# Kernel optimization log

Hardware: AMD Instinct MI355X
Metric: run time of the kernel (lower is better)

## Reference

```python
import jax, jax.numpy as jnp
import numpy as np

B, C, T, H, W = 1, 512, 8, 48, 48
GROUPS = 32
EPS = 1e-6


def setup_inputs() -> dict:
    key = jax.random.key(0)
    ks = jax.random.split(key, 6)
    s = 0.02  # init scale for projection weights
    return {
        "x": jax.random.normal(ks[0], (B, C, T, H, W), dtype=jnp.float32),
        "gamma": jnp.ones((C,), dtype=jnp.float32),
        "beta": jnp.zeros((C,), dtype=jnp.float32),
        "wq": jax.random.normal(ks[1], (C, C), dtype=jnp.float32) * s,
        "bq": jnp.zeros((C,), dtype=jnp.float32),
        "wk": jax.random.normal(ks[2], (C, C), dtype=jnp.float32) * s,
        "bk": jnp.zeros((C,), dtype=jnp.float32),
        "wv": jax.random.normal(ks[3], (C, C), dtype=jnp.float32) * s,
        "bv": jnp.zeros((C,), dtype=jnp.float32),
        "wo": jax.random.normal(ks[4], (C, C), dtype=jnp.float32) * s,
        "bo": jnp.zeros((C,), dtype=jnp.float32),
    }


def _group_norm(x, gamma, beta):
    b, c, t, h, w = x.shape
    xg = x.reshape(b, GROUPS, c // GROUPS, t, h, w)
    mu = xg.mean(axis=(2, 3, 4, 5), keepdims=True)
    var = xg.var(axis=(2, 3, 4, 5), keepdims=True)
    xn = ((xg - mu) * jax.lax.rsqrt(var + EPS)).reshape(b, c, t, h, w)
    return xn * gamma[None, :, None, None, None] + beta[None, :, None, None, None]


def _proj(h, wgt, bias):
    # CausalConv3d with kernel_size=1 == pointwise channel linear
    return jnp.einsum('oc,bcthw->bothw', wgt, h) + bias[None, :, None, None, None]


def reference(x, gamma, beta, wq, bq, wk, bk, wv, bv, wo, bo):
    hn = _group_norm(x, gamma, beta)
    q = _proj(hn, wq, bq)
    k = _proj(hn, wk, bk)
    v = _proj(hn, wv, bv)
    b, c, t, h, w = q.shape
    n = h * w
    # per-frame spatial attention: (b, t, n, c)
    qf = q.transpose(0, 2, 3, 4, 1).reshape(b, t, n, c)
    kf = k.transpose(0, 2, 3, 4, 1).reshape(b, t, n, c)
    vf = v.transpose(0, 2, 3, 4, 1).reshape(b, t, n, c)
    scores = jnp.einsum('btqc,btkc->btqk', qf, kf) * (c ** -0.5)
    attn = jax.nn.softmax(scores, axis=-1)
    of = jnp.einsum('btqk,btkc->btqc', attn, vf)
    o = of.reshape(b, t, h, w, c).transpose(0, 4, 1, 2, 3)
    o = _proj(o, wo, bo)
    return x + o
```

## Files before the change

### kernel.cpp

```cpp
#include <hip/hip_runtime.h>
#include <hip/hip_bf16.h>
#include <cstdint>
#include <type_traits>

typedef __attribute__((ext_vector_type(8))) __bf16 bf16x8;
typedef __attribute__((ext_vector_type(4))) float f32x4;
typedef __attribute__((ext_vector_type(2))) long longx2;

struct bf2frag { bf16x8 k0, k1; };

__device__ __forceinline__ float bf2f(unsigned short u) {
  union { uint32_t i; float f; } v; v.i = (uint32_t)u << 16; return v.f;
}
__device__ __forceinline__ unsigned short f2bf(float f) {
  union { float f; uint32_t i; } v{f};
  uint32_t r = v.i + 0x7fffu + ((v.i >> 16) & 1u);
  return (unsigned short)(r >> 16);
}

__device__ __forceinline__ void gll(const void* g, void* l) {
  __builtin_amdgcn_global_load_lds(
      (const __attribute__((address_space(1))) uint32_t*)(uintptr_t)g,
      (__attribute__((address_space(3))) uint32_t*)(uint32_t)(uintptr_t)l,
      16, 0, 0);
}

__device__ __forceinline__ void bar() {
  asm volatile("" ::: "memory");
  __builtin_amdgcn_s_barrier();
  asm volatile("" ::: "memory");
}

#define VMCNT(n) asm volatile("s_waitcnt vmcnt(" #n ")" ::: "memory")

template <int N>
__device__ __forceinline__ void vmw() {
  if constexpr (N == 0) { VMCNT(0); }
  else if constexpr (N == 1) { VMCNT(1); }
  else if constexpr (N == 2) { VMCNT(2); }
  else if constexpr (N == 3) { VMCNT(3); }
  else if constexpr (N == 4) { VMCNT(4); }
  else if constexpr (N == 5) { VMCNT(5); }
  else if constexpr (N == 6) { VMCNT(6); }
  else if constexpr (N == 7) { VMCNT(7); }
  else if constexpr (N == 8) { VMCNT(8); }
  else if constexpr (N == 9) { VMCNT(9); }
  else if constexpr (N == 10) { VMCNT(10); }
  else { VMCNT(12); }
}

__device__ __forceinline__ f32x4 mma(bf16x8 a, bf16x8 b, f32x4 c) {
  return __builtin_amdgcn_mfma_f32_16x16x32_bf16(a, b, c, 0, 0, 0);
}
__device__ __forceinline__ f32x4 mma(long a, long b, f32x4 c) {
  return __builtin_amdgcn_mfma_f32_16x16x32_fp8_fp8(a, b, c, 0, 0, 0);
}
__device__ __forceinline__ f32x4 mmak(const bf2frag& a, const bf2frag& b, f32x4 c, int k2) {
  return k2 ? mma(a.k1, b.k1, c) : mma(a.k0, b.k0, c);
}
__device__ __forceinline__ f32x4 mmak(longx2 a, longx2 b, f32x4 c, int k2) {
  return mma(a[k2], b[k2], c);
}

__device__ __forceinline__ int perm64(int m) {
  return (m & ~63) | (((m >> 3) & 3) << 4) | (((m >> 5) & 1) << 3) | (m & 7);
}

__global__ __launch_bounds__(256) void stats_partial_k(const float* __restrict__ x,
                                                       float* __restrict__ part) {
  const int g = blockIdx.x >> 3, p = blockIdx.x & 7;
  const float* base = x + (long)g * 16 * 18432 + (long)p * 2304;
  float s = 0.f, ss = 0.f;
  for (int idx = threadIdx.x; idx < 16 * 576; idx += 256) {
    const int c = idx / 576, i4 = idx % 576;
    const float4 v = *(const float4*)(base + (long)c * 18432 + i4 * 4);
    s += v.x + v.y + v.z + v.w;
    ss += v.x * v.x + v.y * v.y + v.z * v.z + v.w * v.w;
  }
  __shared__ float rs[256], rss[256];
  rs[threadIdx.x] = s; rss[threadIdx.x] = ss;
  __syncthreads();
  for (int o = 128; o > 0; o >>= 1) {
    if ((int)threadIdx.x < o) { rs[threadIdx.x] += rs[threadIdx.x + o]; rss[threadIdx.x] += rss[threadIdx.x + o]; }
    __syncthreads();
  }
  if (threadIdx.x == 0) { part[blockIdx.x * 2] = rs[0]; part[blockIdx.x * 2 + 1] = rss[0]; }
}

__global__ __launch_bounds__(256) void gn_transpose_k(const float* __restrict__ x,
                                                      const float* __restrict__ part,
                                                      const float* __restrict__ gamma,
                                                      const float* __restrict__ beta,
                                                      unsigned short* __restrict__ hnT) {
  __shared__ float tile[64][65];
  __shared__ float sm[4], sr[4];
  const int c0 = blockIdx.x * 64, n0 = blockIdx.y * 64;
  const int tn = threadIdx.x & 63, tr = threadIdx.x >> 6;
  if (threadIdx.x < 4) {
    const int g = (c0 >> 4) + threadIdx.x;
    float s = 0.f, ss = 0.f;
    for (int p = 0; p < 8; ++p) { s += part[(g * 8 + p) * 2]; ss += part[(g * 8 + p) * 2 + 1]; }
    const float mean = s / 294912.0f;
    const float var = ss / 294912.0f - mean * mean;
    sm[threadIdx.x] = mean;
    sr[threadIdx.x] = rsqrtf(var + 1e-6f);
  }
  __syncthreads();
  for (int cc = tr; cc < 64; cc += 4) {
    const int c = c0 + cc;
    const float mean = sm[cc >> 4], rstd = sr[cc >> 4];
    const float v = x[(long)c * 18432 + n0 + tn];
    tile[cc][tn] = (v - mean) * rstd * gamma[c] + beta[c];
  }
  __syncthreads();
  for (int nn = tr; nn < 64; nn += 4) {
    hnT[(long)(n0 + nn) * 512 + c0 + tn] = f2bf(tile[tn][nn]);
  }
}

__global__ __launch_bounds__(256) void pack4_bf16_k(const float* __restrict__ w0,
                                                    const float* __restrict__ w1,
                                                    const float* __restrict__ w2,
                                                    const float* __restrict__ w3,
                                                    unsigned short* __restrict__ o0,
                                                    unsigned short* __restrict__ o1,
                                                    unsigned short* __restrict__ o2,
                                                    unsigned short* __restrict__ o3,
                                                    const float* __restrict__ bq,
                                                    const float* __restrict__ bk,
                                                    float* __restrict__ bqk) {
  const int y = blockIdx.y;
  if (y == 4) {
    if (blockIdx.x == 0) {
      const int i = threadIdx.x * 4;
#pragma unroll
      for (int j = 0; j < 4; ++j) {
        const int t = i + j;
        bqk[t] = (t < 512) ? bq[t] : bk[t - 512];
      }
    }
    return;
  }
  const float* w = (y == 0) ? w0 : (y == 1) ? w1 : (y == 2) ? w2 : w3;
  unsigned short* o = (y == 0) ? o0 : (y == 1) ? o1 : (y == 2) ? o2 : o3;
  const int i = (blockIdx.x * 256 + threadIdx.x) * 4;
  const float4 v = *(const float4*)(w + i);
  ushort4 u; u.x = f2bf(v.x); u.y = f2bf(v.y); u.z = f2bf(v.z); u.w = f2bf(v.w);
  *(ushort4*)(o + i) = u;
}

template <int BM, int BIAS_MODE, int OUT_MODE, int STATS, int SCALEN, int MODE, int FP8, int P2,
          int WL = 0, int KU = 1>
__global__ __launch_bounds__((BM == 256) ? 512 : 256, (WL && FP8) ? (KU == 2 ? 2 : 4) : 2)
void gemm256(const void* __restrict__ A, long lda, long sAz,
             const void* __restrict__ B, long ldb, long sBz,
             void* __restrict__ Cp, long ldc, long sCz,
             const float* __restrict__ bias,
             const float* __restrict__ resid,
             float* __restrict__ rowsums,
             const float* __restrict__ linv,
             float alpha, int K, int gx, int gy) {
  static_assert(KU == 1 || FP8, "KU=2 only on fp8 path");
  constexpr int EB = FP8 ? 1 : 2;
  constexpr int THREADS = (BM == 256) ? 512 : 256;
  constexpr int BN = WL ? 128 : 256;
  constexpr int BK = 64 * KU;
  constexpr int HBA = (BM / 2) * BK * EB;
  constexpr int HBB = (BN / 2) * BK * EB;
  constexpr int HBA0 = HBA / KU, HBB0 = HBB / KU;
  constexpr int GA = HBA / (THREADS * 16);
  constexpr int GB = HBB / (THREADS * 16);
  constexpr int GA0 = GA / KU, GB0 = GB / KU;
  constexpr int V0 = GB + 2 * GA, V3 = 2 * GB + GA, VP = GB + GA;
  constexpr int NSLOT = WL ? 8 : ((BM == 256) ? 8 : 4);
  constexpr int NSLOTP = NSLOT + 1;
  constexpr int MR = WL ? 4 : 8;
  constexpr int FQ = WL ? 2 : 4;
  constexpr int PRIO = !P2;
  __shared__ alignas(16) unsigned char As[2][2][HBA];
  __shared__ alignas(16) unsigned char Bs[2][2][HBB];
  __shared__ float linvs[SCALEN == 2 ? BN : 1];
  using ABt2 = typename std::conditional<FP8, longx2, bf2frag>::type;

  const int tid = threadIdx.x;
  const int lane = tid & 63, wid = tid >> 6;
  const int wm = WL ? (wid >> 1) : ((BM == 256) ? (wid & 1) : 0);
  const int wn = WL ? (wid & 1) : ((BM == 256) ? (wid >> 1) : wid);
  int bx, by, bz;
  const void* Asel = A;
  const void* Bsel = B;
  void* Csel = Cp;
  const float* biasSel = bias;
  long ldcSel = ldc;
  bool bias_m = (BIAS_MODE == 1);
  {
    const int g8 = blockIdx.x & 7, n = blockIdx.x >> 3;
    if (MODE == 0) { bz = g8; bx = n % gx; by = n / gx; }
    else if (MODE == 1) { bz = 0; bx = n % gx; by = g8 * gy + n / gx; }
    else if (MODE == 2) { bz = 0; by = n % gy; bx = g8 * gx + n / gy; }
    else {
      bz = 0;
      if ((int)blockIdx.x < gx) {
        bx = n % 8; by = g8 * 18 + n / 8;
      } else {
        const int b2 = (int)blockIdx.x - gx;
        const int g82 = b2 & 7, n2 = b2 >> 3;
        by = n2 % 4; bx = g82 * 18 + n2 / 4;
        Asel = B;
        Bsel = (const void*)resid;
        Csel = (void*)rowsums;
        biasSel = linv;
        ldcSel = 18432;
        bias_m = false;
      }
    }
  }
  const unsigned char* Ab = (const unsigned char*)Asel + ((long)bz * sAz + (long)bx * BM * lda) * EB;
  const unsigned char* Bb = (const unsigned char*)Bsel + ((long)bz * sBz + (long)by * BN * ldb) * EB;

  if constexpr (SCALEN == 2) {
    if (tid < BN) {
      const int ntile = K / BN;
      float L = 0.f;
      for (int xx = 0; xx < ntile; ++xx)
        L += rowsums[((long)(bz * ntile + xx)) * K + by * BN + tid];
      linvs[tid] = 1.0f / L;
    }
  }

  auto stageA = [&](int slot, int h, int k0) {
    if constexpr (!FP8) {
      const int ksw = ((tid & 7) << 3) ^ (((tid >> 3) & 7) << 3);
#pragma unroll
      for (int call = 0; call < GA; ++call) {
        const int r = call * (THREADS / 8) + (tid >> 3);
        const int grow = WL ? (((r >> 5) << 6) + h * 32 + (r & 31))
                            : (((r >> 6) << 7) + h * 64 + (r & 63));
        gll(Ab + ((long)grow * lda + k0) * 2 + ksw * 2, &As[slot][h][call * THREADS * 16 + tid * 16]);
      }
    } else {
#pragma unroll
      for (int call = 0; call < GA; ++call) {
        const int sub = call / GA0, c0 = call % GA0;
        const int l = c0 * (THREADS / 4) + (tid >> 2);
        const int grow = WL ? (((l >> 5) << 6) + h * 32 + (l & 31))
                            : (((l >> 6) << 7) + h * 64 + (l & 63));
        const int x = (((l & 3) ^ ((l >> 2) & 3)) << 4);
        gll(Ab + (long)grow * lda + k0 + sub * 64 + (((tid & 3) << 4) ^ x),
            &As[slot][h][call * THREADS * 16 + tid * 16]);
      }
    }
  };
  auto stageB = [&](int slot, int h, int k0) {
    if constexpr (!FP8) {
      const int ksw = ((tid & 7) << 3) ^ (((tid >> 3) & 7) << 3);
#pragma unroll
      for (int call = 0; call < GB; ++call) {
        const int r = call * (THREADS / 8) + (tid >> 3);
        const int grow = ((r >> 5) << 6) + h * 32 + (r & 31);
        gll(Bb + ((long)grow * ldb + k0) * 2 + ksw * 2, &Bs[slot][h][call * THREADS * 16 + tid * 16]);
      }
    } else {
#pragma unroll
      for (int call = 0; call < GB; ++call) {
        const int sub = call / GB0, c0 = call % GB0;
        const int l = c0 * (THREADS / 4) + (tid >> 2);
        const int grow = ((l >> 5) << 6) + h * 32 + (l & 31);
        const int x = (((l & 3) ^ ((l >> 2) & 3)) << 4);
        gll(Bb + (long)grow * ldb + k0 + sub * 64 + (((tid & 3) << 4) ^ x),
            &Bs[slot][h][call * THREADS * 16 + tid * 16]);
      }
    }
  };
  auto ldA = [&](int slot, int mh, int fq, int sub) -> ABt2 {
    const int r = (WL ? wm * 32 : wm * 64) + fq * 16 + (lane & 15);
    if constexpr (!FP8) {
      bf2frag f;
      const int kk0 = (((lane >> 4) << 3)) ^ ((r & 7) << 3);
      const int kk1 = (32 + ((lane >> 4) << 3)) ^ ((r & 7) << 3);
      f.k0 = *reinterpret_cast<const bf16x8*>(&As[slot][mh][r * 128 + kk0 * 2]);
      f.k1 = *reinterpret_cast<const bf16x8*>(&As[slot][mh][r * 128 + kk1 * 2]);
      return f;
    } else {
      const int x = (((r & 3) ^ ((r >> 2) & 3)) << 4);
      const int kk = ((lane >> 4) << 4) ^ x;
      return *reinterpret_cast<const longx2*>(&As[slot][mh][sub * HBA0 + r * 64 + kk]);
    }
  };
  auto ldB = [&](int slot, int nh, int g, int sub) -> ABt2 {
    const int r = wn * 32 + g * 16 + (lane & 15);
    if constexpr (!FP8) {
      bf2frag f;
      const int kk0 = (((lane >> 4) << 3)) ^ ((r & 7) << 3);
      const int kk1 = (32 + ((lane >> 4) << 3)) ^ ((r & 7) << 3);
      f.k0 = *reinterpret_cast<const bf16x8*>(&Bs[slot][nh][r * 128 + kk0 * 2]);
      f.k1 = *reinterpret_cast<const bf16x8*>(&Bs[slot][nh][r * 128 + kk1 * 2]);
      return f;
    } else {
      const int x = (((r & 3) ^ ((r >> 2) & 3)) << 4);
      const int kk = ((lane >> 4) << 4) ^ x;
      return *reinterpret_cast<const longx2*>(&Bs[slot][nh][sub * HBB0 + r * 64 + kk]);
    }
  };

  f32x4 acc[MR][4] = {};
  ABt2 a[FQ * KU], b0[2 * KU], b1[2 * KU];

#define READ_A(SLOT, MH)                                                       \
  _Pragma("unroll") for (int fq = 0; fq < FQ; ++fq)                            \
    _Pragma("unroll") for (int sub = 0; sub < KU; ++sub)                       \
      a[fq * KU + sub] = ldA(SLOT, MH, fq, sub);
#define READ_B(SLOT, NH, DST)                                                  \
  _Pragma("unroll") for (int g = 0; g < 2; ++g)                                \
    _Pragma("unroll") for (int sub = 0; sub < KU; ++sub)                       \
      DST[g * KU + sub] = ldB(SLOT, NH, g, sub);
#define MFMA_QUAD(MH, NH, BARR)                                                \
  if constexpr (PRIO) __builtin_amdgcn_s_setprio(1);                           \
  _Pragma("unroll") for (int fq = 0; fq < FQ; ++fq)                            \
    _Pragma("unroll") for (int g = 0; g < 2; ++g)                              \
      _Pragma("unroll") for (int sub = 0; sub < KU; ++sub)                     \
        _Pragma("unroll") for (int k2 = 0; k2 < 2; ++k2)                       \
          acc[(MH) * FQ + fq][(NH) * 2 + g] =                                  \
              mmak(a[fq * KU + sub], BARR[g * KU + sub],                       \
                   acc[(MH) * FQ + fq][(NH) * 2 + g], k2);                     \
  if constexpr (PRIO) __builtin_amdgcn_s_setprio(0);

  const int KT = K / BK;
  stageB(0, 0, 0);
  stageA(0, 0, 0);
  stageB(0, 1, 0);
  stageA(0, 1, 0);
  stageB(1, 0, BK);
  if constexpr (!P2) stageA(1, 1, BK);
  vmw<VP>();
  bar();

  if constexpr (!P2) {
    for (int W = 0; W < KT; ++W) {
      const int s = W & 1;
      const int kn1 = (W + 1) * BK, kn2 = (W + 2) * BK;
      const bool st1 = (W + 1 < KT), st2 = (W + 2 < KT);
      READ_A(s, 0)
      READ_B(s, 0, b0)
      if (st1) stageA(s ^ 1, 0, kn1);
      bar();
      MFMA_QUAD(0, 0, b0)
      if (st1) { vmw<V0>(); }
      bar();
      READ_B(s, 1, b1)
      if (st1) stageB(s ^ 1, 1, kn1);
      bar();
      MFMA_QUAD(0, 1, b1)
      bar();
      READ_A(s, 1)
      if (st2) stageB(s, 0, kn2);
      bar();
      MFMA_QUAD(1, 1, b1)
      bar();
      if (st2) stageA(s, 1, kn2);
      bar();
      MFMA_QUAD(1, 0, b0)
      if (st2) { vmw<V3>(); } else { vmw<0>(); }
      bar();
    }
  } else {
    for (int W = 0; W < KT; ++W) {
      const int s = W & 1;
      const int kn1 = (W + 1) * BK, kn2 = (W + 2) * BK;
      const bool st1 = (W + 1 < KT), st2 = (W + 2 < KT);
      READ_A(s, 0)
      READ_B(s, 0, b0)
      READ_B(s, 1, b1)
      if (st1) { stageA(s ^ 1, 0, kn1); stageB(s ^ 1, 1, kn1); stageA(s ^ 1, 1, kn1); }
      bar();
      MFMA_QUAD(0, 0, b0)
      MFMA_QUAD(0, 1, b1)
      if (st1) { vmw<2 * (GA + GB)>(); } else { vmw<0>(); }
      bar();
      READ_A(s, 1)
      if (st2) stageB(s, 0, kn2);
      bar();
      MFMA_QUAD(1, 1, b1)
      MFMA_QUAD(1, 0, b0)
      if (st2) { vmw<GA + GB>(); } else if (st1) { vmw<GA>(); } else { vmw<0>(); }
      bar();
    }
  }

  const int mg0 = bx * BM + (WL ? wm * 64 : wm * 128) + ((lane >> 4) << 2);
  const int ng0 = by * BN + wn * 64 + (lane & 15);
  float* red = (float*)&As[0][0][0];
#pragma unroll
  for (int N = 0; N < 4; ++N) {
    const int n = ng0 + (N >> 1) * 32 + (N & 1) * 16;
    float bn;
    if constexpr (MODE == 3) bn = bias_m ? 0.f : biasSel[n];
    else bn = (BIAS_MODE == 2) ? bias[n] : 0.f;
    const float sc = (SCALEN == 1) ? linv[(long)bz * 2304 + n]
                   : (SCALEN == 2) ? linvs[n - by * BN] : 1.0f;
    float eN = 0.f;
#pragma unroll
    for (int M = 0; M < MR; ++M) {
      const int m = mg0 + (WL ? ((M >> 1) * 32 + (M & 1) * 16) : ((M >> 2) * 64 + (M & 3) * 16));
      const f32x4 av = acc[M][N];
      float vals[4];
#pragma unroll
      for (int j = 0; j < 4; ++j) {
        float addv;
        if constexpr (MODE == 3) addv = bias_m ? biasSel[m + j] : bn;
        else if constexpr (BIAS_MODE == 1) addv = bias[m + j];
        else addv = bn;
        vals[j] = av[j] * alpha + addv;
        if (SCALEN) vals[j] *= sc;
        if (STATS) { vals[j] = __expf(vals[j]); eN += vals[j]; }
      }
      if (OUT_MODE == 0) {
        ushort4 o; o.x = f2bf(vals[0]); o.y = f2bf(vals[1]); o.z = f2bf(vals[2]); o.w = f2bf(vals[3]);
        *(ushort4*)((unsigned short*)Csel + (long)bz * sCz + (long)n * ldcSel + m) = o;
      } else if (OUT_MODE == 2) {
        int pk = __builtin_amdgcn_cvt_pk_fp8_f32(vals[0], vals[1], 0, false);
        pk = __builtin_amdgcn_cvt_pk_fp8_f32(vals[2], vals[3], pk, true);
        *(int*)((unsigned char*)Csel + (long)bz * sCz + (long)n * ldcSel + perm64(m)) = pk;
      } else {
        const float* rp = resid + (long)n * ldcSel + m;
        float4 o; o.x = vals[0] + rp[0]; o.y = vals[1] + rp[1]; o.z = vals[2] + rp[2]; o.w = vals[3] + rp[3];
        *(float4*)((float*)Csel + (long)bz * sCz + (long)n * ldcSel + m) = o;
      }
    }
    if (STATS) {
      const int nloc = wn * 64 + (N >> 1) * 32 + (N & 1) * 16 + (lane & 15);
      const int slot = wm * 4 + (lane >> 4);
      red[nloc * NSLOTP + slot] = eN;
    }
  }
  if (STATS) {
    bar();
    if (tid < BN) {
      float L = 0.f;
#pragma unroll
      for (int s2 = 0; s2 < NSLOT; ++s2) L += red[tid * NSLOTP + s2];
      rowsums[((long)(bz * gx + bx)) * 2304 + by * BN + tid] = L;
    }
  }
#undef READ_A
#undef READ_B
#undef MFMA_QUAD
}

extern "C" void kernel_launch(void* const* d_in, const int* in_sizes, int n_in,
                              void* d_out, int out_size, void* d_ws, size_t ws_size,
                              hipStream_t stream) {
  const float* x = (const float*)d_in[0];
  const float* gamma = (const float*)d_in[1];
  const float* beta = (const float*)d_in[2];
  const float* wq = (const float*)d_in[3];
  const float* bq = (const float*)d_in[4];
  const float* wk = (const float*)d_in[5];
  const float* bk = (const float*)d_in[6];
  const float* wv = (const float*)d_in[7];
  const float* bv = (const float*)d_in[8];
  const float* wo = (const float*)d_in[9];
  const float* bo = (const float*)d_in[10];
  float* out = (float*)d_out;

  char* ws = (char*)d_ws;
  size_t off = 0;
  auto alloc = [&](size_t bytes) {
    char* p = ws + off;
    off = (off + bytes + 255) & ~(size_t)255;
    return p;
  };
  float* part = (float*)alloc(256 * 2 * sizeof(float));
  unsigned short* wqkb = (unsigned short*)alloc((size_t)2 * 262144 * 2);
  unsigned short* wvb = (unsigned short*)alloc((size_t)262144 * 2);
  unsigned short* wob = (unsigned short*)alloc((size_t)262144 * 2);
  float* bqk = (float*)alloc(1024 * sizeof(float));
  float* rowsums = (float*)alloc((size_t)8 * 18 * 2304 * sizeof(float));
  unsigned short* hnT = (unsigned short*)alloc((size_t)18432 * 512 * 2);
  unsigned char* qkA = (unsigned char*)alloc((size_t)18432 * 1024);
  unsigned char* vT = (unsigned char*)alloc((size_t)512 * 18432);
  unsigned char* Sm = (unsigned char*)alloc((size_t)8 * 2304 * 2304);
  unsigned short* Ob = hnT;
  (void)ws_size; (void)in_sizes; (void)n_in; (void)out_size;

  stats_partial_k<<<dim3(256), dim3(256), 0, stream>>>(x, part);
  gn_transpose_k<<<dim3(8, 288), dim3(256), 0, stream>>>(x, part, gamma, beta, hnT);
  pack4_bf16_k<<<dim3(256, 5), dim3(256), 0, stream>>>(wq, wk, wv, wo,
                                                       wqkb, wqkb + 262144, wvb, wob,
                                                       bq, bk, bqk);

  gemm256<128, 1, 2, 0, 0, 3, 0, 1, 1><<<dim3(1728), dim3(256), 0, stream>>>(
      wqkb, 512, 0, hnT, 512, 0, (void*)qkA, 1024, 0, bqk,
      (const float*)wvb, (float*)vT, bv, 1.0f, 512, 1152, 0);
  gemm256<128, 0, 2, 1, 0, 0, 1, 1, 1><<<dim3(2592), dim3(256), 0, stream>>>(
      qkA + 512, 1024, (long)2304 * 1024, qkA, 1024, (long)2304 * 1024, (void*)Sm, 2304,
      (long)2304 * 2304, nullptr, nullptr, rowsums, nullptr,
      0.044194173824159216f, 512, 18, 18);
  gemm256<128, 0, 0, 0, 2, 0, 1, 1, 1><<<dim3(576), dim3(256), 0, stream>>>(
      vT, 18432, 2304, Sm, 2304, (long)2304 * 2304, (void*)Ob, 512, (long)2304 * 512,
      nullptr, nullptr, rowsums, nullptr, 1.0f, 2304, 4, 18);
  gemm256<128, 2, 1, 0, 0, 2, 0, 1, 1><<<dim3(576), dim3(256), 0, stream>>>(
      Ob, 512, 0, wob, 512, 0, (void*)out, 18432, 0, bo, x, nullptr, nullptr,
      1.0f, 512, 18, 4);
}
```

Measured before the change: 214.9 us.

## Add 8-wave WL=2 layout for QKV projection GEMM splitting N across waves

Adds a WL=2 variant of the GEMM kernel that uses 512 threads (8 waves) per 128x128 tile, with each wave owning a 32-column slice instead of 64, halving per-wave accumulators and B fragment loads. The QKV projection GEMM launch is switched to this variant. The intent is more waves per tile for better latency hiding and lower register pressure. The cost is more LDS reads of A per wave relative to compute and more barrier participants. Staging counts per thread also change with the thread count.

After: 210.6 us. -2.0%, faster.

```diff
diff --git a/kernel.cpp b/kernel.cpp
--- a/kernel.cpp
+++ b/kernel.cpp
@@ -151,7 +151,7 @@
 
 template <int BM, int BIAS_MODE, int OUT_MODE, int STATS, int SCALEN, int MODE, int FP8, int P2,
           int WL = 0, int KU = 1>
-__global__ __launch_bounds__((BM == 256) ? 512 : 256, (WL && FP8) ? (KU == 2 ? 2 : 4) : 2)
+__global__ __launch_bounds__((BM == 256 || WL == 2) ? 512 : 256, (WL == 1 && FP8) ? (KU == 2 ? 2 : 4) : 2)
 void gemm256(const void* __restrict__ A, long lda, long sAz,
              const void* __restrict__ B, long ldb, long sBz,
              void* __restrict__ Cp, long ldc, long sCz,
@@ -162,7 +162,7 @@
              float alpha, int K, int gx, int gy) {
   static_assert(KU == 1 || FP8, "KU=2 only on fp8 path");
   constexpr int EB = FP8 ? 1 : 2;
-  constexpr int THREADS = (BM == 256) ? 512 : 256;
+  constexpr int THREADS = (BM == 256 || WL == 2) ? 512 : 256;
   constexpr int BN = WL ? 128 : 256;
   constexpr int BK = 64 * KU;
   constexpr int HBA = (BM / 2) * BK * EB;
@@ -175,6 +175,7 @@
   constexpr int NSLOT = WL ? 8 : ((BM == 256) ? 8 : 4);
   constexpr int NSLOTP = NSLOT + 1;
   constexpr int MR = WL ? 4 : 8;
+  constexpr int NR = (WL == 2) ? 2 : 4;
   constexpr int FQ = WL ? 2 : 4;
   constexpr int PRIO = !P2;
   __shared__ alignas(16) unsigned char As[2][2][HBA];
@@ -184,8 +185,8 @@
 
   const int tid = threadIdx.x;
   const int lane = tid & 63, wid = tid >> 6;
-  const int wm = WL ? (wid >> 1) : ((BM == 256) ? (wid & 1) : 0);
-  const int wn = WL ? (wid & 1) : ((BM == 256) ? (wid >> 1) : wid);
+  const int wm = (WL == 2) ? (wid >> 2) : (WL ? (wid >> 1) : ((BM == 256) ? (wid & 1) : 0));
+  const int wn = (WL == 2) ? (wid & 3) : (WL ? (wid & 1) : ((BM == 256) ? (wid >> 1) : wid));
   int bx, by, bz;
   const void* Asel = A;
   const void* Bsel = B;
@@ -288,22 +289,23 @@
     }
   };
   auto ldB = [&](int slot, int nh, int g, int sub) -> ABt2 {
-    const int r = wn * 32 + g * 16 + (lane & 15);
+    const int half = (WL == 2) ? (wn & 1) : nh;
+    const int r = ((WL == 2) ? (wn >> 1) : wn) * 32 + g * 16 + (lane & 15);
     if constexpr (!FP8) {
       bf2frag f;
       const int kk0 = (((lane >> 4) << 3)) ^ ((r & 7) << 3);
       const int kk1 = (32 + ((lane >> 4) << 3)) ^ ((r & 7) << 3);
-      f.k0 = *reinterpret_cast<const bf16x8*>(&Bs[slot][nh][r * 128 + kk0 * 2]);
-      f.k1 = *reinterpret_cast<const bf16x8*>(&Bs[slot][nh][r * 128 + kk1 * 2]);
+      f.k0 = *reinterpret_cast<const bf16x8*>(&Bs[slot][half][r * 128 + kk0 * 2]);
+      f.k1 = *reinterpret_cast<const bf16x8*>(&Bs[slot][half][r * 128 + kk1 * 2]);
       return f;
     } else {
       const int x = (((r & 3) ^ ((r >> 2) & 3)) << 4);
       const int kk = ((lane >> 4) << 4) ^ x;
-      return *reinterpret_cast<const longx2*>(&Bs[slot][nh][sub * HBB0 + r * 64 + kk]);
+      return *reinterpret_cast<const longx2*>(&Bs[slot][half][sub * HBB0 + r * 64 + kk]);
     }
   };
 
-  f32x4 acc[MR][4] = {};
+  f32x4 acc[MR][NR] = {};
   ABt2 a[FQ * KU], b0[2 * KU], b1[2 * KU];
 
 #define READ_A(SLOT, MH)                                                       \
@@ -370,17 +372,17 @@
       const bool st1 = (W + 1 < KT), st2 = (W + 2 < KT);
       READ_A(s, 0)
       READ_B(s, 0, b0)
-      READ_B(s, 1, b1)
+      if constexpr (WL != 2) { READ_B(s, 1, b1) }
       if (st1) { stageA(s ^ 1, 0, kn1); stageB(s ^ 1, 1, kn1); stageA(s ^ 1, 1, kn1); }
       bar();
       MFMA_QUAD(0, 0, b0)
-      MFMA_QUAD(0, 1, b1)
+      if constexpr (WL != 2) { MFMA_QUAD(0, 1, b1) }
       if (st1) { vmw<2 * (GA + GB)>(); } else { vmw<0>(); }
       bar();
       READ_A(s, 1)
       if (st2) stageB(s, 0, kn2);
       bar();
-      MFMA_QUAD(1, 1, b1)
+      if constexpr (WL != 2) { MFMA_QUAD(1, 1, b1) }
       MFMA_QUAD(1, 0, b0)
       if (st2) { vmw<GA + GB>(); } else if (st1) { vmw<GA>(); } else { vmw<0>(); }
       bar();
@@ -388,11 +390,11 @@
   }
 
   const int mg0 = bx * BM + (WL ? wm * 64 : wm * 128) + ((lane >> 4) << 2);
-  const int ng0 = by * BN + wn * 64 + (lane & 15);
+  const int ng0 = by * BN + ((WL == 2) ? wn * 32 : wn * 64) + (lane & 15);
   float* red = (float*)&As[0][0][0];
 #pragma unroll
-  for (int N = 0; N < 4; ++N) {
-    const int n = ng0 + (N >> 1) * 32 + (N & 1) * 16;
+  for (int N = 0; N < NR; ++N) {
+    const int n = ng0 + ((WL == 2) ? N * 16 : ((N >> 1) * 32 + (N & 1) * 16));
     float bn;
     if constexpr (MODE == 3) bn = bias_m ? 0.f : biasSel[n];
     else bn = (BIAS_MODE == 2) ? bias[n] : 0.f;
@@ -428,7 +430,7 @@
       }
     }
     if (STATS) {
-      const int nloc = wn * 64 + (N >> 1) * 32 + (N & 1) * 16 + (lane & 15);
+      const int nloc = n - by * BN;
       const int slot = wm * 4 + (lane >> 4);
       red[nloc * NSLOTP + slot] = eN;
     }
@@ -489,7 +491,7 @@
                                                        wqkb, wqkb + 262144, wvb, wob,
                                                        bq, bk, bqk);
 
-  gemm256<128, 1, 2, 0, 0, 3, 0, 1, 1><<<dim3(1728), dim3(256), 0, stream>>>(
+  gemm256<128, 1, 2, 0, 0, 3, 0, 1, 2><<<dim3(1728), dim3(512), 0, stream>>>(
       wqkb, 512, 0, hnT, 512, 0, (void*)qkA, 1024, 0, bqk,
       (const float*)wvb, (float*)vT, bv, 1.0f, 512, 1152, 0);
   gemm256<128, 0, 2, 1, 0, 0, 1, 1, 1><<<dim3(2592), dim3(256), 0, stream>>>(
```
